# Optimization experiments

Measured on AMD Instinct MI355X. Metric: run time of the kernel, lower is better.

## Reference

```python
import jax, jax.numpy as jnp
import numpy as np

B, INDIM, ENC, BOT, DEC = 2048, 20000, 512, 128, 512
EPS = 1e-5


def _bn(x, g, b):
    # BatchNorm1d in training mode: biased batch stats
    m = jnp.mean(x, axis=0)
    v = jnp.mean(jnp.square(x - m), axis=0)
    return (x - m) * jax.lax.rsqrt(v + EPS) * g + b


def setup_inputs() -> dict:
    key = jax.random.key(0)
    ks = jax.random.split(key, 8)
    s = 0.02  # small init scale keeps exp() outputs finite
    return {
        "x": jax.random.uniform(ks[0], (B, INDIM), dtype=jnp.float32),
        "bn0_g": jnp.ones((INDIM,), jnp.float32),
        "bn0_b": jnp.zeros((INDIM,), jnp.float32),
        "enc_W": jax.random.normal(ks[1], (ENC, INDIM), jnp.float32) * s,
        "enc_b": jnp.zeros((ENC,), jnp.float32),
        "bn1_g": jnp.ones((ENC,), jnp.float32),
        "bn1_b": jnp.zeros((ENC,), jnp.float32),
        "bot_W": jax.random.normal(ks[2], (BOT, ENC), jnp.float32) * s,
        "bot_b": jnp.zeros((BOT,), jnp.float32),
        "bn2_g": jnp.ones((BOT,), jnp.float32),
        "bn2_b": jnp.zeros((BOT,), jnp.float32),
        "dec_W": jax.random.normal(ks[3], (DEC, BOT), jnp.float32) * s,
        "dec_b": jnp.zeros((DEC,), jnp.float32),
        "o1_W": jax.random.normal(ks[4], (INDIM, DEC), jnp.float32) * s,
        "o1_b": jnp.zeros((INDIM,), jnp.float32),
        "o2_W": jax.random.normal(ks[5], (INDIM, DEC), jnp.float32) * s,
        "o2_b": jnp.zeros((INDIM,), jnp.float32),
        "o3_W": jax.random.normal(ks[6], (INDIM, DEC), jnp.float32) * s,
        "o3_b": jnp.zeros((INDIM,), jnp.float32),
    }


def reference(x, bn0_g, bn0_b, enc_W, enc_b, bn1_g, bn1_b, bot_W, bot_b,
              bn2_g, bn2_b, dec_W, dec_b, o1_W, o1_b, o2_W, o2_b, o3_W, o3_b):
    # row-sum / median normalization; diag-inverse @ x == x / s[:, None]
    row_sum = jnp.sum(x, axis=1)                     # [B]
    s = row_sum / jnp.median(row_sum)                # [B]
    h = jnp.log1p(x / s[:, None])                    # log(inv(diag(s)) @ x + 1)
    h = _bn(h, bn0_g, bn0_b)
    h = jax.nn.relu(h @ enc_W.T + enc_b)
    h = _bn(h, bn1_g, bn1_b)
    h = jax.nn.relu(h @ bot_W.T + bot_b)
    h = _bn(h, bn2_g, bn2_b)
    h = jax.nn.relu(h @ dec_W.T + dec_b)
    M = jnp.exp(h @ o1_W.T + o1_b)
    M_loss = s[:, None] * M                          # diag(s) @ M
    pai = jax.nn.sigmoid(h @ o2_W.T + o2_b)
    theta = jnp.exp(h @ o3_W.T + o3_b)
    return pai, M, theta, M_loss
```

## Files before the change

### kernel.cpp

```cpp
#include <hip/hip_runtime.h>
#include <hip/hip_bf16.h>
#include <math.h>

#define B_    2048
#define IND   20000
#define ENCN  512
#define BOTN  128
#define DECN  512
#define KP1   20480
#define NP    20224
#define SPLITK 16
#define KSTEP1 20
#define BNEPS 1e-5f

typedef __hip_bfloat16 bf16;
typedef __bf16 bf16x8 __attribute__((ext_vector_type(8)));
typedef float f32x4 __attribute__((ext_vector_type(4)));
typedef unsigned short u16;

__device__ __forceinline__ u16 f2bfu(float f) {
  __hip_bfloat16 h = __float2bfloat16(f);
  return *reinterpret_cast<u16*>(&h);
}

__device__ __forceinline__ void gload_lds16(const bf16* g, bf16* l) {
  __builtin_amdgcn_global_load_lds(
      (const __attribute__((address_space(1))) void*)g,
      (__attribute__((address_space(3))) void*)l, 16, 0, 0);
}

__global__ void rowsum_k(const float* __restrict__ x, float* __restrict__ row_sum) {
  const int row = blockIdx.x;
  const f32x4* xr = (const f32x4*)(x + (size_t)row * IND);
  float s = 0.f;
  for (int i = threadIdx.x; i < IND / 4; i += 256) {
    f32x4 v = xr[i];
    s += (v[0] + v[1]) + (v[2] + v[3]);
  }
#pragma unroll
  for (int o = 32; o > 0; o >>= 1) s += __shfl_down(s, o, 64);
  __shared__ float ws4[4];
  if ((threadIdx.x & 63) == 0) ws4[threadIdx.x >> 6] = s;
  __syncthreads();
  if (threadIdx.x == 0) row_sum[row] = (ws4[0] + ws4[1]) + (ws4[2] + ws4[3]);
}

__global__ void median_scale_k(const float* __restrict__ row_sum,
                               float* __restrict__ sArr, float* __restrict__ invs) {
  __shared__ float v[B_];
  const int tid = threadIdx.x;
  v[tid] = row_sum[tid];
  v[tid + 1024] = row_sum[tid + 1024];
  __syncthreads();
  for (int k = 2; k <= B_; k <<= 1) {
    for (int j = k >> 1; j > 0; j >>= 1) {
      for (int i = tid; i < B_; i += 1024) {
        int ixj = i ^ j;
        if (ixj > i) {
          bool up = ((i & k) == 0);
          float a = v[i], b = v[ixj];
          if ((a > b) == up) { v[i] = b; v[ixj] = a; }
        }
      }
      __syncthreads();
    }
  }
  float med = 0.5f * (v[B_ / 2 - 1] + v[B_ / 2]);
  for (int i = tid; i < B_; i += 1024) {
    float rs = row_sum[i];
    sArr[i] = rs / med;
    invs[i] = med / rs;
  }
}

__global__ void pass2_k(const float* __restrict__ x, const float* __restrict__ invs,
                        bf16* __restrict__ L, float* __restrict__ part_s,
                        float* __restrict__ part_q) {
  const int c0 = (blockIdx.x * 256 + threadIdx.x) * 4;
  const int rblk = blockIdx.y;
  const int r0 = rblk * 32;
  const bool valid = (c0 < IND);
  f32x4 sum = {0.f, 0.f, 0.f, 0.f}, sq = {0.f, 0.f, 0.f, 0.f};
  for (int r = r0; r < r0 + 32; ++r) {
    f32x4 lv = {0.f, 0.f, 0.f, 0.f};
    if (valid) {
      f32x4 v = *(const f32x4*)(x + (size_t)r * IND + c0);
      float iv = invs[r];
      lv[0] = log1pf(v[0] * iv); lv[1] = log1pf(v[1] * iv);
      lv[2] = log1pf(v[2] * iv); lv[3] = log1pf(v[3] * iv);
      sum += lv; sq += lv * lv;
    }
    ushort4 o;
    o.x = f2bfu(lv[0]); o.y = f2bfu(lv[1]); o.z = f2bfu(lv[2]); o.w = f2bfu(lv[3]);
    *(ushort4*)((u16*)L + (size_t)r * KP1 + c0) = o;
  }
  if (valid) {
    *(f32x4*)(part_s + (size_t)rblk * KP1 + c0) = sum;
    *(f32x4*)(part_q + (size_t)rblk * KP1 + c0) = sq;
  }
}

__global__ void finalize_bn_k(const float* __restrict__ part_s, const float* __restrict__ part_q,
                              const float* __restrict__ g, const float* __restrict__ b,
                              float* __restrict__ scale, float* __restrict__ shift) {
  int c = blockIdx.x * 256 + threadIdx.x;
  if (c >= IND) return;
  float s = 0.f, q = 0.f;
  for (int z = 0; z < 64; ++z) {
    s += part_s[(size_t)z * KP1 + c];
    q += part_q[(size_t)z * KP1 + c];
  }
  const float invN = 1.f / (float)B_;
  float mean = s * invN;
  float var = q * invN - mean * mean;
  float sc = g[c] * rsqrtf(var + BNEPS);
  scale[c] = sc;
  shift[c] = b[c] - mean * sc;
}

__global__ void prepw_k(const float* __restrict__ encW, const float* __restrict__ enc_b,
                        const float* __restrict__ scale0, const float* __restrict__ shift0,
                        bf16* __restrict__ Wp, float* __restrict__ bias1) {
  const int e = blockIdx.x;
  float local = 0.f;
  for (int j0 = threadIdx.x * 4; j0 < KP1; j0 += 1024) {
    ushort4 o;
    if (j0 < IND) {
      f32x4 w = *(const f32x4*)(encW + (size_t)e * IND + j0);
      f32x4 sc = *(const f32x4*)(scale0 + j0);
      f32x4 sh = *(const f32x4*)(shift0 + j0);
      local += sh[0] * w[0] + sh[1] * w[1] + sh[2] * w[2] + sh[3] * w[3];
      o.x = f2bfu(w[0] * sc[0]); o.y = f2bfu(w[1] * sc[1]);
      o.z = f2bfu(w[2] * sc[2]); o.w = f2bfu(w[3] * sc[3]);
    } else {
      o.x = 0; o.y = 0; o.z = 0; o.w = 0;
    }
    *(ushort4*)((u16*)Wp + (size_t)e * KP1 + j0) = o;
  }
#pragma unroll
  for (int o = 32; o > 0; o >>= 1) local += __shfl_down(local, o, 64);
  __shared__ float red[4];
  if ((threadIdx.x & 63) == 0) red[threadIdx.x >> 6] = local;
  __syncthreads();
  if (threadIdx.x == 0) bias1[e] = enc_b[e] + ((red[0] + red[1]) + (red[2] + red[3]));
}

template <int MODE>
__global__ __launch_bounds__(512, 2)
void gemm256(const bf16* __restrict__ A, const bf16* __restrict__ Bm,
             int Kpad, int ksteps,
             float* __restrict__ out0, float* __restrict__ out1,
             const float* __restrict__ bias, const float* __restrict__ sArr,
             int ldo, int Nlimit) {
  extern __shared__ __align__(16) bf16 smem[];
  bf16* AsB = smem;
  bf16* BsB = smem + 32768;
  const int tid = threadIdx.x;
  const int lane = tid & 63;
  const int wave = tid >> 6;
  const int wr = wave >> 2;
  const int wc = wave & 3;

  const int nwg = gridDim.x;
  const int q8 = nwg >> 3;
  const int bid = blockIdx.x;
  const int swz = (bid & 7) * q8 + (bid >> 3);
  const int xm = swz & 7;
  const int rest = swz >> 3;
  int yn, z;
  if (MODE == 0) { yn = rest & 1; z = rest >> 1; } else { yn = rest; z = 0; }
  const int m0 = xm * 256;
  const int n0 = yn * 256;
  const int kbeg = z * ksteps * 64;

  const int srow = tid >> 3;
  const int schunk = (tid & 7) ^ (srow & 7);
  const bf16* gA = A + (size_t)(m0 + srow) * Kpad + kbeg + schunk * 8;
  const bf16* gB = Bm + (size_t)(n0 + srow) * Kpad + kbeg + schunk * 8;
  const int ldst = tid * 8;

  f32x4 acc[8][4] = {};
  const int lrow = lane & 15;
  const int kq = lane >> 4;

  auto STAGE = [&](int ks, int buf) {
    const bf16* ga = gA + (size_t)ks * 64;
    const bf16* gb = gB + (size_t)ks * 64;
    bf16* la = AsB + buf * 16384 + ldst;
    bf16* lb = BsB + buf * 16384 + ldst;
#pragma unroll
    for (int i = 0; i < 4; ++i) {
      gload_lds16(ga + (size_t)(i * 64) * Kpad, la + i * 4096);
      gload_lds16(gb + (size_t)(i * 64) * Kpad, lb + i * 4096);
    }
  };

  STAGE(0, 0);
  asm volatile("s_waitcnt vmcnt(0)" ::: "memory");
  __builtin_amdgcn_s_barrier();

  int cur = 0;
  for (int ks = 0; ks < ksteps; ++ks) {
    if (ks + 1 < ksteps) STAGE(ks + 1, cur ^ 1);
    const bf16* As = AsB + cur * 16384;
    const bf16* Bs = BsB + cur * 16384;
#pragma unroll
    for (int kk = 0; kk < 2; ++kk) {
      const int kc = kk * 4 + kq;
      bf16x8 af[8], bfv[4];
#pragma unroll
      for (int m = 0; m < 8; ++m) {
        const int row = wr * 128 + m * 16 + lrow;
        af[m] = *(const bf16x8*)(&As[row * 64 + ((kc ^ (row & 7)) << 3)]);
      }
#pragma unroll
      for (int n = 0; n < 4; ++n) {
        const int row = wc * 64 + n * 16 + lrow;
        bfv[n] = *(const bf16x8*)(&Bs[row * 64 + ((kc ^ (row & 7)) << 3)]);
      }
#pragma unroll
      for (int m = 0; m < 8; ++m)
#pragma unroll
        for (int n = 0; n < 4; ++n)
          acc[m][n] = __builtin_amdgcn_mfma_f32_16x16x32_bf16(bfv[n], af[m], acc[m][n], 0, 0, 0);
    }
    if (ks + 1 < ksteps) {
      asm volatile("s_waitcnt vmcnt(0)" ::: "memory");
      __builtin_amdgcn_s_barrier();
      cur ^= 1;
    }
  }

  float* o0 = out0;
  if (MODE == 0) o0 += (size_t)z * ((size_t)B_ * ldo);
  const int growb = m0 + wr * 128 + lrow;
  const int gcolb = n0 + wc * 64 + kq * 4;
#pragma unroll
  for (int m = 0; m < 8; ++m) {
    const int grow = growb + m * 16;
    float srow_s = 0.f;
    if (MODE == 2) srow_s = sArr[grow];
#pragma unroll
    for (int n = 0; n < 4; ++n) {
      const int gcol = gcolb + n * 16;
      f32x4 v = acc[m][n];
      if (MODE == 0) {
        *(f32x4*)(&o0[(size_t)grow * ldo + gcol]) = v;
      } else if (gcol < Nlimit) {
        f32x4 bb = *(const f32x4*)(&bias[gcol]);
        f32x4 t = v + bb;
        f32x4 r;
        if (MODE == 1) {
#pragma unroll
          for (int j = 0; j < 4; ++j) r[j] = 1.f / (1.f + __expf(-t[j]));
          *(f32x4*)(&o0[(size_t)grow * ldo + gcol]) = r;
        } else if (MODE == 2) {
#pragma unroll
          for (int j = 0; j < 4; ++j) r[j] = __expf(t[j]);
          *(f32x4*)(&o0[(size_t)grow * ldo + gcol]) = r;
          f32x4 rl;
#pragma unroll
          for (int j = 0; j < 4; ++j) rl[j] = srow_s * r[j];
          *(f32x4*)(&out1[(size_t)grow * ldo + gcol]) = rl;
        } else {
#pragma unroll
          for (int j = 0; j < 4; ++j) r[j] = __expf(t[j]);
          *(f32x4*)(&o0[(size_t)grow * ldo + gcol]) = r;
        }
      }
    }
  }
}

template <int MODE>
__global__ __launch_bounds__(256, 2)
void gemm128(const bf16* __restrict__ A, const bf16* __restrict__ Bm,
             int Kpad, int ksteps,
             float* __restrict__ outF, bf16* __restrict__ outB,
             const float* __restrict__ bias, int ldo) {
  __shared__ __align__(16) bf16 As[2][128 * 64];
  __shared__ __align__(16) bf16 Bs[2][128 * 64];
  const int tid = threadIdx.x;
  const int wave = tid >> 6;
  const int lane = tid & 63;
  const int wr = wave >> 1, wc = wave & 1;
  const int m0 = blockIdx.x * 128;
  const int n0 = blockIdx.y * 128;

  const int srow = wave * 32 + (lane >> 3);
  const int scol = ((lane & 7) ^ (lane >> 3)) * 8;
  const bf16* gA = A + (size_t)(m0 + srow) * Kpad + scol;
  const bf16* gB = Bm + (size_t)(n0 + srow) * Kpad + scol;
  const int lbase = wave * 2048;

  f32x4 acc[4][4] = {};
  const int lrow = lane & 15;
  const int swz = lrow & 7;
  const int kq = lane >> 4;

  auto STAGE = [&](int ks, int buf) {
    const bf16* ga = gA + (size_t)ks * 64;
    const bf16* gb = gB + (size_t)ks * 64;
#pragma unroll
    for (int i = 0; i < 4; ++i) {
      gload_lds16(ga + (size_t)(i * 8) * Kpad, &As[buf][lbase + i * 512]);
      gload_lds16(gb + (size_t)(i * 8) * Kpad, &Bs[buf][lbase + i * 512]);
    }
  };

  STAGE(0, 0);
  asm volatile("s_waitcnt vmcnt(0)" ::: "memory");
  __builtin_amdgcn_s_barrier();

  int cur = 0;
  for (int ks = 0; ks < ksteps; ++ks) {
    if (ks + 1 < ksteps) STAGE(ks + 1, cur ^ 1);
#pragma unroll
    for (int kk = 0; kk < 2; ++kk) {
      const int kc = kk * 4 + kq;
      bf16x8 af[4], bfv[4];
#pragma unroll
      for (int m = 0; m < 4; ++m) {
        const int row = wr * 64 + m * 16 + lrow;
        af[m] = *(const bf16x8*)(&As[cur][row * 64 + (((kc ^ swz) & 7) << 3)]);
      }
#pragma unroll
      for (int n = 0; n < 4; ++n) {
        const int row = wc * 64 + n * 16 + lrow;
        bfv[n] = *(const bf16x8*)(&Bs[cur][row * 64 + (((kc ^ swz) & 7) << 3)]);
      }
#pragma unroll
      for (int m = 0; m < 4; ++m)
#pragma unroll
        for (int n = 0; n < 4; ++n)
          acc[m][n] = __builtin_amdgcn_mfma_f32_16x16x32_bf16(bfv[n], af[m], acc[m][n], 0, 0, 0);
    }
    if (ks + 1 < ksteps) {
      asm volatile("s_waitcnt vmcnt(0)" ::: "memory");
      __builtin_amdgcn_s_barrier();
      cur ^= 1;
    }
  }

  const int growb = m0 + wr * 64 + lrow;
  const int gcolb = n0 + wc * 64 + kq * 4;
#pragma unroll
  for (int m = 0; m < 4; ++m) {
    const int grow = growb + m * 16;
#pragma unroll
    for (int n = 0; n < 4; ++n) {
      const int gcol = gcolb + n * 16;
      f32x4 bb = *(const f32x4*)(&bias[gcol]);
      f32x4 t = acc[m][n] + bb;
      if (MODE == 4) {
        f32x4 r;
#pragma unroll
        for (int j = 0; j < 4; ++j) r[j] = fmaxf(t[j], 0.f);
        *(f32x4*)(&outF[(size_t)grow * ldo + gcol]) = r;
      } else {
        ushort4 o;
        o.x = f2bfu(fmaxf(t[0], 0.f)); o.y = f2bfu(fmaxf(t[1], 0.f));
        o.z = f2bfu(fmaxf(t[2], 0.f)); o.w = f2bfu(fmaxf(t[3], 0.f));
        *(ushort4*)((u16*)outB + (size_t)grow * ldo + gcol) = o;
      }
    }
  }
}

__global__ void reduce1_k(const float* __restrict__ Cp, const float* __restrict__ bias1,
                          float* __restrict__ C1) {
  const size_t i4 = ((size_t)blockIdx.x * 256 + threadIdx.x) * 4;
  f32x4 t = {0.f, 0.f, 0.f, 0.f};
#pragma unroll
  for (int z = 0; z < SPLITK; ++z) t += *(const f32x4*)(Cp + (size_t)z * (B_ * ENCN) + i4);
  f32x4 bb = *(const f32x4*)(bias1 + (i4 & (ENCN - 1)));
  t += bb;
  f32x4 r;
#pragma unroll
  for (int j = 0; j < 4; ++j) r[j] = fmaxf(t[j], 0.f);
  *(f32x4*)(C1 + i4) = r;
}

__global__ void colpart_k(const float* __restrict__ X, int C,
                          float* __restrict__ ps, float* __restrict__ pq) {
  const int cl = threadIdx.x & 63;
  const int rg = threadIdx.x >> 6;
  const int c = blockIdx.x * 64 + cl;
  const int r0 = blockIdx.y * 64 + rg * 16;
  float sum = 0.f, sq = 0.f;
  for (int rr = 0; rr < 16; ++rr) {
    float v = X[(size_t)(r0 + rr) * C + c];
    sum += v; sq += v * v;
  }
  __shared__ float ls[4][64], lq[4][64];
  ls[rg][cl] = sum; lq[rg][cl] = sq;
  __syncthreads();
  if (rg == 0) {
    sum = (ls[0][cl] + ls[1][cl]) + (ls[2][cl] + ls[3][cl]);
    sq = (lq[0][cl] + lq[1][cl]) + (lq[2][cl] + lq[3][cl]);
    ps[(size_t)blockIdx.y * C + c] = sum;
    pq[(size_t)blockIdx.y * C + c] = sq;
  }
}

__global__ void colfin_k(const float* __restrict__ ps, const float* __restrict__ pq,
                         const float* __restrict__ g, const float* __restrict__ b,
                         float* __restrict__ scale, float* __restrict__ shift, int C) {
  int c = blockIdx.x * 256 + threadIdx.x;
  if (c >= C) return;
  float sum = 0.f, sq = 0.f;
  for (int z = 0; z < 32; ++z) {
    sum += ps[(size_t)z * C + c];
    sq += pq[(size_t)z * C + c];
  }
  const float invN = 1.f / (float)B_;
  float mean = sum * invN;
  float var = sq * invN - mean * mean;
  float sc = g[c] * rsqrtf(var + BNEPS);
  scale[c] = sc;
  shift[c] = b[c] - mean * sc;
}

__global__ void affine_k(const float* __restrict__ X, const float* __restrict__ sc,
                         const float* __restrict__ sh, bf16* __restrict__ out, int Cm1) {
  const size_t i4 = ((size_t)blockIdx.x * 256 + threadIdx.x) * 4;
  const int c0 = (int)(i4 & (size_t)Cm1);
  f32x4 v = *(const f32x4*)(X + i4);
  f32x4 s = *(const f32x4*)(sc + c0);
  f32x4 h = *(const f32x4*)(sh + c0);
  f32x4 t = v * s + h;
  ushort4 o;
  o.x = f2bfu(t[0]); o.y = f2bfu(t[1]); o.z = f2bfu(t[2]); o.w = f2bfu(t[3]);
  *(ushort4*)((u16*)out + i4) = o;
}

__global__ void cvtw_k(const float* __restrict__ src, bf16* __restrict__ dst) {
  const size_t i4 = ((size_t)blockIdx.x * 256 + threadIdx.x) * 4;
  f32x4 v = *(const f32x4*)(src + i4);
  ushort4 o;
  o.x = f2bfu(v[0]); o.y = f2bfu(v[1]); o.z = f2bfu(v[2]); o.w = f2bfu(v[3]);
  *(ushort4*)((u16*)dst + i4) = o;
}

__global__ void cvt_o_k(const float* __restrict__ Wsrc, bf16* __restrict__ Wb) {
  const size_t idx = ((size_t)blockIdx.x * 256 + threadIdx.x) * 4;
  const int e = (int)(idx >> 9);
  ushort4 o;
  if (e < IND) {
    f32x4 v = *(const f32x4*)(Wsrc + idx);
    o.x = f2bfu(v[0]); o.y = f2bfu(v[1]); o.z = f2bfu(v[2]); o.w = f2bfu(v[3]);
  } else {
    o.x = 0; o.y = 0; o.z = 0; o.w = 0;
  }
  *(ushort4*)((u16*)Wb + idx) = o;
}

extern "C" void kernel_launch(void* const* d_in, const int* in_sizes, int n_in,
                              void* d_out, int out_size, void* d_ws, size_t ws_size,
                              hipStream_t stream) {
  const float* x     = (const float*)d_in[0];
  const float* bn0_g = (const float*)d_in[1];
  const float* bn0_b = (const float*)d_in[2];
  const float* enc_W = (const float*)d_in[3];
  const float* enc_b = (const float*)d_in[4];
  const float* bn1_g = (const float*)d_in[5];
  const float* bn1_b = (const float*)d_in[6];
  const float* bot_W = (const float*)d_in[7];
  const float* bot_b = (const float*)d_in[8];
  const float* bn2_g = (const float*)d_in[9];
  const float* bn2_b = (const float*)d_in[10];
  const float* dec_W = (const float*)d_in[11];
  const float* dec_b = (const float*)d_in[12];
  const float* o1_W  = (const float*)d_in[13];
  const float* o1_b  = (const float*)d_in[14];
  const float* o2_W  = (const float*)d_in[15];
  const float* o2_b  = (const float*)d_in[16];
  const float* o3_W  = (const float*)d_in[17];
  const float* o3_b  = (const float*)d_in[18];

  char* wsb = (char*)d_ws;
  size_t off = 0;
  auto alloc = [&](size_t bytes) -> void* {
    void* p = wsb + off;
    off = (off + bytes + 255) & ~(size_t)255;
    return p;
  };
  float* row_sum = (float*)alloc(B_ * 4);
  float* sArr    = (float*)alloc(B_ * 4);
  float* invs    = (float*)alloc(B_ * 4);
  float* scale0  = (float*)alloc(IND * 4);
  float* shift0  = (float*)alloc(IND * 4);
  float* bias1   = (float*)alloc(ENCN * 4);
  float* scale1  = (float*)alloc(ENCN * 4);
  float* shift1  = (float*)alloc(ENCN * 4);
  float* scale2  = (float*)alloc(BOTN * 4);
  float* shift2  = (float*)alloc(BOTN * 4);
  float* ps1     = (float*)alloc(32 * ENCN * 4);
  float* pq1     = (float*)alloc(32 * ENCN * 4);
  float* ps2     = (float*)alloc(32 * BOTN * 4);
  float* pq2     = (float*)alloc(32 * BOTN * 4);
  float* C1      = (float*)alloc((size_t)B_ * ENCN * 4);
  float* C2f     = (float*)alloc((size_t)B_ * BOTN * 4);
  float* Cp      = (float*)alloc((size_t)SPLITK * B_ * ENCN * 4);
  bf16*  L       = (bf16*)alloc((size_t)B_ * KP1 * 2);
  bf16*  Wp      = (bf16*)alloc((size_t)ENCN * KP1 * 2);
  bf16*  A1b     = (bf16*)alloc((size_t)B_ * ENCN * 2);
  bf16*  A2b     = (bf16*)alloc((size_t)B_ * BOTN * 2);
  bf16*  botWb   = (bf16*)alloc((size_t)BOTN * ENCN * 2);
  bf16*  decWb   = (bf16*)alloc((size_t)DECN * BOTN * 2);
  bf16*  h3      = (bf16*)alloc((size_t)B_ * DECN * 2);
  bf16*  wbf0    = (bf16*)alloc((size_t)NP * 512 * 2);
  bf16*  wbf1    = (bf16*)alloc((size_t)NP * 512 * 2);
  bf16*  wbf2    = (bf16*)alloc((size_t)NP * 512 * 2);
  float* part_s  = Cp;
  float* part_q  = Cp + (size_t)64 * KP1;

  hipFuncSetAttribute(reinterpret_cast<const void*>(gemm256<0>),
                      hipFuncAttributeMaxDynamicSharedMemorySize, 131072);
  hipFuncSetAttribute(reinterpret_cast<const void*>(gemm256<1>),
                      hipFuncAttributeMaxDynamicSharedMemorySize, 131072);
  hipFuncSetAttribute(reinterpret_cast<const void*>(gemm256<2>),
                      hipFuncAttributeMaxDynamicSharedMemorySize, 131072);
  hipFuncSetAttribute(reinterpret_cast<const void*>(gemm256<3>),
                      hipFuncAttributeMaxDynamicSharedMemorySize, 131072);

  rowsum_k<<<B_, 256, 0, stream>>>(x, row_sum);
  median_scale_k<<<1, 1024, 0, stream>>>(row_sum, sArr, invs);

  pass2_k<<<dim3(KP1 / 1024, 64), 256, 0, stream>>>(x, invs, L, part_s, part_q);
  finalize_bn_k<<<(IND + 255) / 256, 256, 0, stream>>>(part_s, part_q, bn0_g, bn0_b,
                                                       scale0, shift0);

  prepw_k<<<ENCN, 256, 0, stream>>>(enc_W, enc_b, scale0, shift0, Wp, bias1);

  gemm256<0><<<8 * 2 * SPLITK, 512, 131072, stream>>>(
      L, Wp, KP1, KSTEP1, Cp, nullptr, nullptr, nullptr, ENCN, ENCN);
  reduce1_k<<<(B_ * ENCN) / 1024, 256, 0, stream>>>(Cp, bias1, C1);

  colpart_k<<<dim3(ENCN / 64, 32), 256, 0, stream>>>(C1, ENCN, ps1, pq1);
  colfin_k<<<2, 256, 0, stream>>>(ps1, pq1, bn1_g, bn1_b, scale1, shift1, ENCN);
  affine_k<<<(B_ * ENCN) / 1024, 256, 0, stream>>>(C1, scale1, shift1, A1b, ENCN - 1);
  cvtw_k<<<(BOTN * ENCN) / 1024, 256, 0, stream>>>(bot_W, botWb);
  gemm128<4><<<dim3(16, 1), 256, 0, stream>>>(A1b, botWb, ENCN, ENCN / 64,
                                              C2f, nullptr, bot_b, BOTN);
  colpart_k<<<dim3(BOTN / 64, 32), 256, 0, stream>>>(C2f, BOTN, ps2, pq2);
  colfin_k<<<1, 256, 0, stream>>>(ps2, pq2, bn2_g, bn2_b, scale2, shift2, BOTN);
  affine_k<<<(B_ * BOTN) / 1024, 256, 0, stream>>>(C2f, scale2, shift2, A2b, BOTN - 1);
  cvtw_k<<<(DECN * BOTN) / 1024, 256, 0, stream>>>(dec_W, decWb);
  gemm128<5><<<dim3(16, 4), 256, 0, stream>>>(A2b, decWb, BOTN, BOTN / 64,
                                              nullptr, h3, dec_b, DECN);

  const int cvtg = (NP * 512) / 1024;
  cvt_o_k<<<cvtg, 256, 0, stream>>>(o1_W, wbf0);
  cvt_o_k<<<cvtg, 256, 0, stream>>>(o2_W, wbf1);
  cvt_o_k<<<cvtg, 256, 0, stream>>>(o3_W, wbf2);

  float* out = (float*)d_out;
  const size_t OFF = (size_t)B_ * IND;
  const int onwg = 8 * (NP / 256);
  gemm256<1><<<onwg, 512, 131072, stream>>>(
      h3, wbf1, 512, 8, out, nullptr, o2_b, nullptr, IND, IND);
  gemm256<2><<<onwg, 512, 131072, stream>>>(
      h3, wbf0, 512, 8, out + OFF, out + 3 * OFF, o1_b, sArr, IND, IND);
  gemm256<3><<<onwg, 512, 131072, stream>>>(
      h3, wbf2, 512, 8, out + 2 * OFF, nullptr, o3_b, nullptr, IND, IND);
}
```

Baseline: 677.1 us.

## Restructure GEMM main loop into fine-grained interleaved load/compute pipeline

The 256x256 GEMM k-loop is rewritten into a two-k-tile-per-iteration schedule. Global-to-LDS loads are split into half-tile stages and interleaved with four MFMA sub-phases separated by barriers, and waitcnt is relaxed to vmcnt(6) so loads stay in flight. It also adds s_setprio around the MFMA blocks and remaps wave rows so each wave reads interleaved 16-row slices. The goal is to hide global load latency and LDS read stalls behind matrix math. The cost is many more barriers per k-step, and the loop now assumes ksteps is even.

```diff
diff --git a/kernel.cpp b/kernel.cpp
--- a/kernel.cpp
+++ b/kernel.cpp
@@ -153,8 +153,8 @@
              const float* __restrict__ bias, const float* __restrict__ sArr,
              int ldo, int Nlimit) {
   extern __shared__ __align__(16) bf16 smem[];
-  bf16* AsB = smem;
-  bf16* BsB = smem + 32768;
+  bf16* Asm = smem;
+  bf16* Bsm = smem + 32768;
   const int tid = threadIdx.x;
   const int lane = tid & 63;
   const int wave = tid >> 6;
@@ -177,67 +177,121 @@
   const int schunk = (tid & 7) ^ (srow & 7);
   const bf16* gA = A + (size_t)(m0 + srow) * Kpad + kbeg + schunk * 8;
   const bf16* gB = Bm + (size_t)(n0 + srow) * Kpad + kbeg + schunk * 8;
-  const int ldst = tid * 8;
-
-  f32x4 acc[8][4] = {};
+  const int dst1 = tid * 8;
+
   const int lrow = lane & 15;
   const int kq = lane >> 4;
-
-  auto STAGE = [&](int ks, int buf) {
-    const bf16* ga = gA + (size_t)ks * 64;
-    const bf16* gb = gB + (size_t)ks * 64;
-    bf16* la = AsB + buf * 16384 + ldst;
-    bf16* lb = BsB + buf * 16384 + ldst;
-#pragma unroll
-    for (int i = 0; i < 4; ++i) {
-      gload_lds16(ga + (size_t)(i * 64) * Kpad, la + i * 4096);
-      gload_lds16(gb + (size_t)(i * 64) * Kpad, lb + i * 4096);
-    }
+  const int rsw = lrow & 7;
+
+  f32x4 acc[8][4] = {};
+  bf16x8 bfv[4][2];
+
+  auto SA = [&](int kt, int half) {
+    const bf16* g = gA + (size_t)(half * 128) * Kpad + (size_t)kt * 64;
+    bf16* l = Asm + (((kt & 1) * 2 + half) << 13) + dst1;
+    gload_lds16(g, l);
+    gload_lds16(g + (size_t)64 * Kpad, l + 4096);
   };
-
-  STAGE(0, 0);
-  asm volatile("s_waitcnt vmcnt(0)" ::: "memory");
+  auto SB = [&](int kt, int half) {
+    const bf16* g = gB + (size_t)(half * 128) * Kpad + (size_t)kt * 64;
+    bf16* l = Bsm + (((kt & 1) * 2 + half) << 13) + dst1;
+    gload_lds16(g, l);
+    gload_lds16(g + (size_t)64 * Kpad, l + 4096);
+  };
+  auto DSA = [&](int slot, int p, bf16x8 af[2][2]) {
+#pragma unroll
+    for (int i = 0; i < 2; ++i) {
+      const int m = 2 * p + i;
+      const int base = ((slot * 2 + (m >> 2)) * 128 + (m & 3) * 32 + wr * 16 + lrow) * 64;
+#pragma unroll
+      for (int kk = 0; kk < 2; ++kk)
+        af[i][kk] = *(const bf16x8*)(&Asm[base + (((kk * 4 + kq) ^ rsw) << 3)]);
+    }
+  };
+  auto DSB = [&](int slot) {
+#pragma unroll
+    for (int n = 0; n < 4; ++n) {
+      const int base = ((slot * 2 + (wc >> 1)) * 128 + (wc & 1) * 64 + n * 16 + lrow) * 64;
+#pragma unroll
+      for (int kk = 0; kk < 2; ++kk)
+        bfv[n][kk] = *(const bf16x8*)(&Bsm[base + (((kk * 4 + kq) ^ rsw) << 3)]);
+    }
+  };
+  auto MF = [&](int p, bf16x8 af[2][2]) {
+    __builtin_amdgcn_s_setprio(1);
+#pragma unroll
+    for (int i = 0; i < 2; ++i)
+#pragma unroll
+      for (int n = 0; n < 4; ++n)
+#pragma unroll
+        for (int kk = 0; kk < 2; ++kk)
+          acc[2 * p + i][n] = __builtin_amdgcn_mfma_f32_16x16x32_bf16(
+              bfv[n][kk], af[i][kk], acc[2 * p + i][n], 0, 0, 0);
+    __builtin_amdgcn_s_setprio(0);
+  };
+
+  SA(0, 0); SA(0, 1); SB(0, 0); SB(0, 1);
+  SB(1, 0); SB(1, 1); SA(1, 0);
+  asm volatile("s_waitcnt vmcnt(6)" ::: "memory");
   __builtin_amdgcn_s_barrier();
 
-  int cur = 0;
-  for (int ks = 0; ks < ksteps; ++ks) {
-    if (ks + 1 < ksteps) STAGE(ks + 1, cur ^ 1);
-    const bf16* As = AsB + cur * 16384;
-    const bf16* Bs = BsB + cur * 16384;
-#pragma unroll
-    for (int kk = 0; kk < 2; ++kk) {
-      const int kc = kk * 4 + kq;
-      bf16x8 af[8], bfv[4];
-#pragma unroll
-      for (int m = 0; m < 8; ++m) {
-        const int row = wr * 128 + m * 16 + lrow;
-        af[m] = *(const bf16x8*)(&As[row * 64 + ((kc ^ (row & 7)) << 3)]);
-      }
-#pragma unroll
-      for (int n = 0; n < 4; ++n) {
-        const int row = wc * 64 + n * 16 + lrow;
-        bfv[n] = *(const bf16x8*)(&Bs[row * 64 + ((kc ^ (row & 7)) << 3)]);
-      }
-#pragma unroll
-      for (int m = 0; m < 8; ++m)
-#pragma unroll
-        for (int n = 0; n < 4; ++n)
-          acc[m][n] = __builtin_amdgcn_mfma_f32_16x16x32_bf16(bfv[n], af[m], acc[m][n], 0, 0, 0);
-    }
-    if (ks + 1 < ksteps) {
-      asm volatile("s_waitcnt vmcnt(0)" ::: "memory");
-      __builtin_amdgcn_s_barrier();
-      cur ^= 1;
-    }
+  const int iters = ksteps >> 1;
+  for (int t = 0; t < iters; ++t) {
+    const int e = 2 * t;
+    const bool last = (t == iters - 1);
+    bf16x8 af[2][2];
+    DSB(0); DSA(0, 0, af);
+    SA(e + 1, 1);
+    __builtin_amdgcn_s_barrier();
+    MF(0, af);
+    __builtin_amdgcn_s_barrier();
+    DSA(0, 1, af);
+    if (!last) SB(e + 2, 0);
+    __builtin_amdgcn_s_barrier();
+    MF(1, af);
+    __builtin_amdgcn_s_barrier();
+    DSA(0, 2, af);
+    if (!last) SB(e + 2, 1);
+    __builtin_amdgcn_s_barrier();
+    MF(2, af);
+    __builtin_amdgcn_s_barrier();
+    DSA(0, 3, af);
+    if (!last) SA(e + 2, 0);
+    if (last) { asm volatile("s_waitcnt vmcnt(0)" ::: "memory"); }
+    else      { asm volatile("s_waitcnt vmcnt(6)" ::: "memory"); }
+    __builtin_amdgcn_s_barrier();
+    MF(3, af);
+    __builtin_amdgcn_s_barrier();
+    DSB(1); DSA(1, 0, af);
+    if (!last) SA(e + 2, 1);
+    __builtin_amdgcn_s_barrier();
+    MF(0, af);
+    __builtin_amdgcn_s_barrier();
+    DSA(1, 1, af);
+    if (!last) SB(e + 3, 0);
+    __builtin_amdgcn_s_barrier();
+    MF(1, af);
+    __builtin_amdgcn_s_barrier();
+    DSA(1, 2, af);
+    if (!last) SB(e + 3, 1);
+    __builtin_amdgcn_s_barrier();
+    MF(2, af);
+    __builtin_amdgcn_s_barrier();
+    DSA(1, 3, af);
+    if (!last) SA(e + 3, 0);
+    if (last) { asm volatile("s_waitcnt vmcnt(0)" ::: "memory"); }
+    else      { asm volatile("s_waitcnt vmcnt(6)" ::: "memory"); }
+    __builtin_amdgcn_s_barrier();
+    MF(3, af);
+    __builtin_amdgcn_s_barrier();
   }
 
   float* o0 = out0;
   if (MODE == 0) o0 += (size_t)z * ((size_t)B_ * ldo);
-  const int growb = m0 + wr * 128 + lrow;
   const int gcolb = n0 + wc * 64 + kq * 4;
 #pragma unroll
   for (int m = 0; m < 8; ++m) {
-    const int grow = growb + m * 16;
+    const int grow = m0 + m * 32 + wr * 16 + lrow;
     float srow_s = 0.f;
     if (MODE == 2) srow_s = sArr[grow];
 #pragma unroll
```

Result: no change. 670.8 us (median of 2 runs) (-0.9%).
